# Kernel optimization log

Measured on AMD Instinct MI355X. Metric: run time of the kernel, lower is better.

The kernel has to match this reference:

```python
import jax, jax.numpy as jnp
import numpy as np


def setup_inputs() -> dict:
    key = jax.random.key(0)
    A = jax.random.normal(key, (16384, 512), dtype=jnp.float32)
    return {"A": A}


def reference(A) -> jnp.ndarray:
    # Original: M = A @ A.T; return sum(triu(M, k=1)) * 2 / (n*(n-1))
    # Algebraic identity: sum_{i<j} <a_i, a_j> = (||sum_i a_i||^2 - sum_i ||a_i||^2) / 2
    # so mean over the n*(n-1)/2 strict-upper entries is:
    #   (||colsum||^2 - sum(A*A)) / (n*(n-1))
    n = A.shape[0]
    s = jnp.sum(A, axis=0)          # [d] column sums
    total = jnp.dot(s, s)           # ||sum_i a_i||^2 = sum over ALL (i,j) pairs
    sq = jnp.sum(A * A)             # diagonal of Gram: sum_i ||a_i||^2
    denom = jnp.asarray(n * (n - 1), dtype=A.dtype)
    return (total - sq) / denom
```

## Files before the change

kernel.cpp:

```cpp
#include <hip/hip_runtime.h>

#define NROWS  16384
#define NCOLS  512
#define NC4    128
#define BLOCKS 256
#define TPB    1024
#define SLOTS  (TPB / NC4)
#define ITERS  (NROWS / (BLOCKS * SLOTS))

__global__ __launch_bounds__(TPB) void ddc2_pass1(
    const float* __restrict__ A,
    float* __restrict__ colsum,
    float* __restrict__ sqsum)
{
    const int tid  = threadIdx.x;
    const int c4   = tid & (NC4 - 1);
    const int slot = tid >> 7;
    const float4* __restrict__ A4 = (const float4*)A;

    const int base = blockIdx.x * SLOTS + slot;

    float4 s = make_float4(0.f, 0.f, 0.f, 0.f);
    float  sq = 0.f;
#pragma unroll
    for (int k = 0; k < ITERS; ++k) {
        float4 v = A4[(base + k * (BLOCKS * SLOTS)) * NC4 + c4];
        s.x += v.x; s.y += v.y; s.z += v.z; s.w += v.w;
        sq  += v.x * v.x + v.y * v.y + v.z * v.z + v.w * v.w;
    }

    __shared__ float4 lds[TPB];
    lds[tid] = s;
    __syncthreads();
#pragma unroll
    for (int stride = TPB / 2; stride >= NC4; stride >>= 1) {
        if (tid < stride) {
            float4 o = lds[tid + stride];
            float4 m = lds[tid];
            m.x += o.x; m.y += o.y; m.z += o.z; m.w += o.w;
            lds[tid] = m;
        }
        __syncthreads();
    }
    if (tid < NC4) {
        ((float4*)colsum)[blockIdx.x * NC4 + tid] = lds[tid];
    }

#pragma unroll
    for (int off = 32; off; off >>= 1) sq += __shfl_down(sq, off, 64);
    __shared__ float wsum[TPB / 64];
    if ((tid & 63) == 0) wsum[tid >> 6] = sq;
    __syncthreads();
    if (tid == 0) {
        float t = 0.f;
#pragma unroll
        for (int i = 0; i < TPB / 64; ++i) t += wsum[i];
        sqsum[blockIdx.x] = t;
    }
}

__global__ __launch_bounds__(512) void ddc2_pass2(
    const float* __restrict__ colsum,
    const float* __restrict__ sqsum,
    float* __restrict__ out)
{
    const int tid = threadIdx.x;

    float acc = 0.f;
#pragma unroll 8
    for (int b = 0; b < BLOCKS; ++b) {
        acc += colsum[b * NCOLS + tid];
    }
    float total = acc * acc;
    float sq = (tid < BLOCKS) ? sqsum[tid] : 0.f;

#pragma unroll
    for (int off = 32; off; off >>= 1) {
        total += __shfl_down(total, off, 64);
        sq    += __shfl_down(sq,    off, 64);
    }
    __shared__ float t8[8], q8[8];
    if ((tid & 63) == 0) { t8[tid >> 6] = total; q8[tid >> 6] = sq; }
    __syncthreads();
    if (tid == 0) {
        double T = 0.0, Q = 0.0;
#pragma unroll
        for (int i = 0; i < 8; ++i) { T += t8[i]; Q += q8[i]; }
        const double denom = (double)NROWS * (double)(NROWS - 1);
        out[0] = (float)((T - Q) / denom);
    }
}

extern "C" void kernel_launch(void* const* d_in, const int* in_sizes, int n_in,
                              void* d_out, int out_size, void* d_ws, size_t ws_size,
                              hipStream_t stream) {
    const float* A = (const float*)d_in[0];
    float* out = (float*)d_out;

    float* colsum = (float*)d_ws;
    float* sqsum  = colsum + BLOCKS * NCOLS;

    ddc2_pass1<<<BLOCKS, TPB, 0, stream>>>(A, colsum, sqsum);
    ddc2_pass2<<<1, 512, 0, stream>>>(colsum, sqsum, out);
}
```

Baseline: 83.28 us.

## Fuse two-pass reduction into one kernel with atomics and last-block finalize

Replaces the per-block partial-sum buffers and the second reduction kernel with global float atomicAdds into a single 512-column accumulator, a last-block detection counter, and a final reduction done by the last block. A memset of the small workspace is added before the launch. This removes the second kernel launch and the pass over 256x512 partials, but adds 256-way atomic contention per column, a memset launch, and makes the float summation order nondeterministic.

```diff
diff --git a/kernel.cpp b/kernel.cpp
--- a/kernel.cpp
+++ b/kernel.cpp
@@ -8,16 +8,17 @@
 #define SLOTS  (TPB / NC4)
 #define ITERS  (NROWS / (BLOCKS * SLOTS))
 
-__global__ __launch_bounds__(TPB) void ddc2_pass1(
+__global__ __launch_bounds__(TPB) void ddc2_fused(
     const float* __restrict__ A,
     float* __restrict__ colsum,
-    float* __restrict__ sqsum)
+    float* __restrict__ sqsum,
+    unsigned int* __restrict__ counter,
+    float* __restrict__ out)
 {
     const int tid  = threadIdx.x;
     const int c4   = tid & (NC4 - 1);
     const int slot = tid >> 7;
     const float4* __restrict__ A4 = (const float4*)A;
-
     const int base = blockIdx.x * SLOTS + slot;
 
     float4 s = make_float4(0.f, 0.f, 0.f, 0.f);
@@ -42,50 +43,50 @@
         }
         __syncthreads();
     }
-    if (tid < NC4) {
-        ((float4*)colsum)[blockIdx.x * NC4 + tid] = lds[tid];
-    }
 
 #pragma unroll
     for (int off = 32; off; off >>= 1) sq += __shfl_down(sq, off, 64);
     __shared__ float wsum[TPB / 64];
     if ((tid & 63) == 0) wsum[tid >> 6] = sq;
     __syncthreads();
+
+    if (tid < NCOLS) {
+        atomicAdd(&colsum[tid], ((const float*)lds)[tid]);
+    }
     if (tid == 0) {
         float t = 0.f;
 #pragma unroll
         for (int i = 0; i < TPB / 64; ++i) t += wsum[i];
-        sqsum[blockIdx.x] = t;
+        atomicAdd(sqsum, t);
     }
-}
 
-__global__ __launch_bounds__(512) void ddc2_pass2(
-    const float* __restrict__ colsum,
-    const float* __restrict__ sqsum,
-    float* __restrict__ out)
-{
-    const int tid = threadIdx.x;
+    __syncthreads();
+    __shared__ int is_last;
+    if (tid == 0) {
+        unsigned int prev = __hip_atomic_fetch_add(counter, 1u,
+                              __ATOMIC_ACQ_REL, __HIP_MEMORY_SCOPE_AGENT);
+        is_last = (prev == BLOCKS - 1);
+    }
+    __syncthreads();
+    if (!is_last) return;
 
-    float acc = 0.f;
-#pragma unroll 8
-    for (int b = 0; b < BLOCKS; ++b) {
-        acc += colsum[b * NCOLS + tid];
+    float total = 0.f;
+    if (tid < NCOLS) {
+        float v = __hip_atomic_load(&colsum[tid], __ATOMIC_RELAXED,
+                                    __HIP_MEMORY_SCOPE_AGENT);
+        total = v * v;
     }
-    float total = acc * acc;
-    float sq = (tid < BLOCKS) ? sqsum[tid] : 0.f;
-
 #pragma unroll
-    for (int off = 32; off; off >>= 1) {
-        total += __shfl_down(total, off, 64);
-        sq    += __shfl_down(sq,    off, 64);
-    }
-    __shared__ float t8[8], q8[8];
-    if ((tid & 63) == 0) { t8[tid >> 6] = total; q8[tid >> 6] = sq; }
+    for (int off = 32; off; off >>= 1) total += __shfl_down(total, off, 64);
+    __syncthreads();
+    if ((tid & 63) == 0) wsum[tid >> 6] = total;
     __syncthreads();
     if (tid == 0) {
-        double T = 0.0, Q = 0.0;
+        double T = 0.0;
 #pragma unroll
-        for (int i = 0; i < 8; ++i) { T += t8[i]; Q += q8[i]; }
+        for (int i = 0; i < TPB / 64; ++i) T += wsum[i];
+        double Q = (double)__hip_atomic_load(sqsum, __ATOMIC_RELAXED,
+                                             __HIP_MEMORY_SCOPE_AGENT);
         const double denom = (double)NROWS * (double)(NROWS - 1);
         out[0] = (float)((T - Q) / denom);
     }
@@ -98,8 +99,9 @@
     float* out = (float*)d_out;
 
     float* colsum = (float*)d_ws;
-    float* sqsum  = colsum + BLOCKS * NCOLS;
+    float* sqsum  = (float*)((char*)d_ws + 2048);
+    unsigned int* counter = (unsigned int*)((char*)d_ws + 2052);
 
-    ddc2_pass1<<<BLOCKS, TPB, 0, stream>>>(A, colsum, sqsum);
-    ddc2_pass2<<<1, 512, 0, stream>>>(colsum, sqsum, out);
+    hipMemsetAsync(d_ws, 0, 2056, stream);
+    ddc2_fused<<<BLOCKS, TPB, 0, stream>>>(A, colsum, sqsum, counter, out);
 }
```

Result: no change. 81.76 us (-1.8%).
